# Kernel tuning notes

Measured on AMD Instinct MI355X. Metric: run time of the kernel, lower is better.

## Reference

```python
import jax, jax.numpy as jnp
import numpy as np

N_HEAD = 16
N_EMBD = 1024
BLOCK = 2048
B, T = 4, 2048


def setup_inputs() -> dict:
    key = jax.random.key(0)
    ks = jax.random.split(key, 5)
    s = 0.02
    return {
        "x": jax.random.normal(ks[0], (B, T, N_EMBD), dtype=jnp.float32),
        "qkv_w": jax.random.normal(ks[1], (3 * N_EMBD, N_EMBD), dtype=jnp.float32) * s,
        "qkv_b": jnp.zeros((3 * N_EMBD,), dtype=jnp.float32),
        "proj_w": jax.random.normal(ks[2], (N_EMBD, N_EMBD), dtype=jnp.float32) * s,
        "proj_b": jnp.zeros((N_EMBD,), dtype=jnp.float32),
    }


def reference(x, qkv_w, qkv_b, proj_w, proj_b):
    Bx, Tx, C = x.shape
    hd = C // N_HEAD
    qkv = x @ qkv_w.T + qkv_b  # [B,T,3C]
    q, k, v = jnp.split(qkv, 3, axis=-1)
    # [B,T,C] -> [B,H,T,hd]
    def heads(t):
        return t.reshape(Bx, Tx, N_HEAD, hd).transpose(0, 2, 1, 3)
    q, k, v = heads(q), heads(k), heads(v)
    scores = jnp.einsum("bhqd,bhkd->bhqk", q, k) / jnp.sqrt(jnp.float32(hd))
    causal = jnp.tril(jnp.ones((Tx, Tx), dtype=bool))
    scores = jnp.where(causal[None, None, :, :], scores, -jnp.inf)
    attn = jax.nn.softmax(scores, axis=-1)
    out = jnp.einsum("bhqk,bhkd->bhqd", attn, v)
    out = out.transpose(0, 2, 1, 3).reshape(Bx, Tx, C)
    return out @ proj_w.T + proj_b
```

## Files before the change

### kernel.cpp

```cpp
#include <hip/hip_runtime.h>
#include <stdint.h>
#include <math.h>

#define DEVI __device__ __forceinline__

typedef __attribute__((ext_vector_type(8))) short bf16x8;
typedef __attribute__((ext_vector_type(4))) float f32x4;

DEVI unsigned short f2bf(float f) {
  union { float f; unsigned u; } v; v.f = f;
  unsigned u = v.u;
  u += 0x7fffu + ((u >> 16) & 1u);
  return (unsigned short)(u >> 16);
}

DEVI unsigned cvt_pk_bf16(float a, float b) {
  unsigned r;
  asm("v_cvt_pk_bf16_f32 %0, %1, %2" : "=v"(r) : "v"(a), "v"(b));
  return r;
}

DEVI f32x4 mfma16(bf16x8 a, bf16x8 b, f32x4 c) {
  return __builtin_amdgcn_mfma_f32_16x16x32_bf16(a, b, c, 0, 0, 0);
}

DEVI void gld16(const unsigned short* g, unsigned short* l) {
  __builtin_amdgcn_global_load_lds(
      (const __attribute__((address_space(1))) unsigned int*)(uintptr_t)g,
      (__attribute__((address_space(3))) unsigned int*)(unsigned int)(uintptr_t)l,
      16, 0, 0);
}

#define VMCNT(n) asm volatile("s_waitcnt vmcnt(" #n ")" ::: "memory")
#define BAR()                              \
  do {                                     \
    __builtin_amdgcn_s_barrier();          \
    __builtin_amdgcn_sched_barrier(0);     \
  } while (0)

__global__ __launch_bounds__(256) void cvt3_kernel(
    const float* __restrict__ a, unsigned short* __restrict__ oa,
    const float* __restrict__ b, unsigned short* __restrict__ ob,
    const float* __restrict__ c, unsigned short* __restrict__ oc) {
  int bid = blockIdx.x;
  const float* in; unsigned short* out; int i;
  if (bid < 8192)       { in = a; out = oa; i = bid; }
  else if (bid < 11264) { in = b; out = ob; i = bid - 8192; }
  else                  { in = c; out = oc; i = bid - 11264; }
  int idx = (i * 256 + (int)threadIdx.x) * 4;
  float4 v = *(const float4*)(in + idx);
  unsigned lo = f2bf(v.x) | ((unsigned)f2bf(v.y) << 16);
  unsigned hi = f2bf(v.z) | ((unsigned)f2bf(v.w) << 16);
  uint2 o; o.x = lo; o.y = hi;
  *(uint2*)(out + idx) = o;
}

template <int MODE, int NBH>
__global__ __launch_bounds__(512, 2) void gemm8(
    const unsigned short* __restrict__ A, const unsigned short* __restrict__ Bw,
    const float* __restrict__ bias, float* __restrict__ Cf,
    unsigned short* __restrict__ Qo, unsigned short* __restrict__ Ko,
    unsigned short* __restrict__ Vo, int M, int N, int K, int nbx) {
  extern __shared__ unsigned short lds[];
  constexpr int BUFS = 8192 + 4096 * NBH;
  const int tid = threadIdx.x;
  const int lane = tid & 63;
  const int w = tid >> 6;
  const int wm = w >> 2, wn = w & 3;
  const int lr = lane & 15, lq = lane >> 4;

  const int cpx = gridDim.x >> 3;
  const int swz = (blockIdx.x & 7) * cpx + (blockIdx.x >> 3);
  const int bx = swz % nbx, by = swz / nbx;
  const int m0 = by * 256, n0 = bx * (NBH * 128);

  const unsigned short* pa = A + (size_t)(m0 + (lane >> 2)) * K + ((lane & 3) << 3);
  const unsigned short* pb = Bw + (size_t)(n0 + (lane >> 2)) * K + ((lane & 3) << 3);

  f32x4 acc[8][2 * NBH] = {};

  auto sA = [&](int buf, int kt, int c) {
    gld16(pa + (size_t)(c << 4) * K + kt, lds + buf * BUFS + (c << 9));
  };
  auto sB = [&](int buf, int kt, int c) {
    gld16(pb + (size_t)(c << 4) * K + kt, lds + buf * BUFS + 8192 + (c << 9));
  };
  auto stage = [&](int buf, int t) {
    const int kt = t << 5;
    sA(buf, kt, w); sA(buf, kt, 8 + w);
    sB(buf, kt, w);
    if constexpr (NBH == 2) sB(buf, kt, 8 + w);
  };

#define LDA(A_, mh)                                                          \
  _Pragma("unroll") for (int i = 0; i < 4; ++i)                              \
    A_[i] = *(const bf16x8*)(As_ + (wm * 128 + (mh) * 64 + i * 16 + lr) * 32 \
                             + lq * 8);
#define LDB(B_, nh)                                                          \
  _Pragma("unroll") for (int j = 0; j < 2; ++j)                              \
    B_[j] = *(const bf16x8*)(Bs_ + (wn * (NBH * 32) + (nh) * 32 + j * 16     \
                             + lr) * 32 + lq * 8);
#define MM(A_, B_, mh, nh)                                                   \
  __builtin_amdgcn_s_setprio(1);                                             \
  _Pragma("unroll") for (int i = 0; i < 4; ++i)                              \
    _Pragma("unroll") for (int j = 0; j < 2; ++j)                            \
      acc[(mh) * 4 + i][(nh) * 2 + j] =                                      \
          mfma16(A_[i], B_[j], acc[(mh) * 4 + i][(nh) * 2 + j]);             \
  __builtin_amdgcn_s_setprio(0);

  const int NT = K >> 5;
  stage(0, 0); stage(1, 1); stage(2, 2);
  if constexpr (NBH == 2) { VMCNT(8); } else { VMCNT(6); }
  BAR();

  for (int t = 0; t < NT; ++t) {
    if (t + 3 < NT) stage((t + 3) & 3, t + 3);
    const unsigned short* As_ = lds + (t & 3) * BUFS;
    const unsigned short* Bs_ = As_ + 8192;
    bf16x8 af0[4], af1[4], b0[2];
    if constexpr (NBH == 2) {
      bf16x8 b1[2];
      LDA(af0, 0); LDB(b0, 0);
      MM(af0, b0, 0, 0);
      LDB(b1, 1);
      MM(af0, b1, 0, 1);
      LDA(af1, 1);
      MM(af1, b1, 1, 1);
      MM(af1, b0, 1, 0);
    } else {
      LDA(af0, 0); LDB(b0, 0);
      MM(af0, b0, 0, 0);
      LDA(af1, 1);
      MM(af1, b0, 1, 0);
    }
    if (t < NT - 3) {
      if constexpr (NBH == 2) { VMCNT(8); } else { VMCNT(6); }
      BAR();
    } else if (t == NT - 3) {
      if constexpr (NBH == 2) { VMCNT(4); } else { VMCNT(3); }
      BAR();
    } else if (t == NT - 2) {
      VMCNT(0); BAR();
    }
  }
#undef LDA
#undef LDB
#undef MM

#pragma unroll
  for (int mt = 0; mt < 8; ++mt) {
#pragma unroll
    for (int nt = 0; nt < 2 * NBH; ++nt) {
      int n_g = n0 + wn * (NBH * 32) + nt * 16 + lr;
      float bv = bias[n_g];
      if (MODE == 1) {
#pragma unroll
        for (int r = 0; r < 4; ++r) {
          int m_g = m0 + wm * 128 + mt * 16 + lq * 4 + r;
          Cf[(size_t)m_g * N + n_g] = acc[mt][nt][r] + bv;
        }
      } else {
        int which = n_g >> 10;
        int rem = n_g & 1023;
        int h = rem >> 6, d = rem & 63;
        int m_base = m0 + wm * 128 + mt * 16 + lq * 4;
        int b = m_base >> 11, tt = m_base & 2047;
        if (which == 2) {
          uint2 pv;
          pv.x = cvt_pk_bf16(acc[mt][nt][0] + bv, acc[mt][nt][1] + bv);
          pv.y = cvt_pk_bf16(acc[mt][nt][2] + bv, acc[mt][nt][3] + bv);
          *(uint2*)(Vo + (((size_t)(b * 16 + h) * 64 + d) * 2048 + tt)) = pv;
        } else {
          unsigned short* p = (which == 0) ? Qo : Ko;
#pragma unroll
          for (int r = 0; r < 4; ++r) {
            size_t idx = (((size_t)(b * 16 + h) * 2048) + tt + r) * 64 + d;
            p[idx] = f2bf(acc[mt][nt][r] + bv);
          }
        }
      }
    }
  }
}

__global__ __launch_bounds__(512, 2) void attn_kernel(
    const unsigned short* __restrict__ Q, const unsigned short* __restrict__ K,
    const unsigned short* __restrict__ V, unsigned short* __restrict__ Y) {
  constexpr int T = 2048, HD = 64, H = 16;
  __shared__ unsigned short Kt[2][64 * 72];
  __shared__ unsigned short Vt[2][64 * 72];
  __shared__ unsigned short Pt[8][16 * 72];

  const int tid = threadIdx.x;
  const int lane = tid & 63;
  const int w = tid >> 6;
  const int lr = lane & 15, lq = lane >> 4;
  const int pair = blockIdx.x;
  const int h = blockIdx.y;
  const int b = blockIdx.z;
  const size_t bh = (size_t)(b * H + h) * T * HD;
  const float SC = 0.125f * 1.44269504089f;

  const int krow = tid >> 3, kcb = (tid & 7) << 3;

  float4 kr, vr;
  auto load_tile = [&](int jt) {
    const int c0 = jt * 64;
    kr = *(const float4*)(K + bh + (size_t)(c0 + krow) * HD + kcb);
    vr = *(const float4*)(V + bh + (size_t)krow * T + c0 + kcb);
  };
  auto stage = [&](int buf) {
    *(float4*)(&Kt[buf][krow * 72 + kcb]) = kr;
    *(float4*)(&Vt[buf][krow * 72 + kcb]) = vr;
  };

  load_tile(0);

  for (int phase = 0; phase < 2; ++phase) {
    const int qt = phase ? (7 - pair) : pair;
    const int q0 = qt * 256;
    const int nkv = 4 * (qt + 1);
    const int qw = q0 + w * 32;

    bf16x8 qf[2][2];
#pragma unroll
    for (int qs = 0; qs < 2; ++qs)
#pragma unroll
      for (int kb = 0; kb < 2; ++kb)
        qf[qs][kb] = *(const bf16x8*)(Q + bh + (size_t)(qw + qs * 16 + lr) * HD +
                                      kb * 32 + lq * 8);

    f32x4 o[2][4] = {};
    float mi[2] = {-INFINITY, -INFINITY}, li[2] = {0.f, 0.f};

    stage(0);
    load_tile(1);
    __syncthreads();

    for (int jt = 0; jt < nkv; ++jt) {
      const int c0 = jt * 64;
      const int buf = jt & 1;

      if (c0 <= qw + 31) {
        f32x4 s[2][4];
        __builtin_amdgcn_s_setprio(1);
#pragma unroll
        for (int nt = 0; nt < 4; ++nt) {
          bf16x8 kf0 = *(const bf16x8*)(&Kt[buf][(nt * 16 + lr) * 72 + lq * 8]);
          bf16x8 kf1 = *(const bf16x8*)(&Kt[buf][(nt * 16 + lr) * 72 + 32 + lq * 8]);
#pragma unroll
          for (int qs = 0; qs < 2; ++qs) {
            f32x4 z = {};
            z = mfma16(kf0, qf[qs][0], z);
            s[qs][nt] = mfma16(kf1, qf[qs][1], z);
          }
        }
        __builtin_amdgcn_s_setprio(0);
        if (c0 + 63 > qw) {
#pragma unroll
          for (int qs = 0; qs < 2; ++qs) {
            int qg = qw + qs * 16 + lr;
#pragma unroll
            for (int nt = 0; nt < 4; ++nt)
#pragma unroll
              for (int r = 0; r < 4; ++r) {
                int kvg = c0 + nt * 16 + lq * 4 + r;
                if (kvg > qg) s[qs][nt][r] = -INFINITY;
              }
          }
        }
        float mxs[2];
#pragma unroll
        for (int qs = 0; qs < 2; ++qs) {
          float mx = -INFINITY;
#pragma unroll
          for (int nt = 0; nt < 4; ++nt)
            mx = fmaxf(mx, fmaxf(fmaxf(s[qs][nt][0], s[qs][nt][1]),
                                 fmaxf(s[qs][nt][2], s[qs][nt][3])));
          mx = fmaxf(mx, __shfl_xor(mx, 16));
          mx = fmaxf(mx, __shfl_xor(mx, 32));
          mxs[qs] = mx * SC;
        }
        if (!__all((mxs[0] <= mi[0] + 8.f) && (mxs[1] <= mi[1] + 8.f))) {
#pragma unroll
          for (int qs = 0; qs < 2; ++qs) {
            float mnew = fmaxf(mi[qs], mxs[qs]);
            float alpha = __builtin_amdgcn_exp2f(mi[qs] - mnew);
            mi[qs] = mnew;
            li[qs] *= alpha;
#pragma unroll
            for (int nt = 0; nt < 4; ++nt)
#pragma unroll
              for (int r = 0; r < 4; ++r) o[qs][nt][r] *= alpha;
          }
        }
        bf16x8 pf[2][2];
#pragma unroll
        for (int qs = 0; qs < 2; ++qs) {
          float rs = 0.f;
#pragma unroll
          for (int nt = 0; nt < 4; ++nt) {
            float p0 = __builtin_amdgcn_exp2f(fmaf(s[qs][nt][0], SC, -mi[qs]));
            float p1 = __builtin_amdgcn_exp2f(fmaf(s[qs][nt][1], SC, -mi[qs]));
            float p2 = __builtin_amdgcn_exp2f(fmaf(s[qs][nt][2], SC, -mi[qs]));
            float p3 = __builtin_amdgcn_exp2f(fmaf(s[qs][nt][3], SC, -mi[qs]));
            rs += (p0 + p1) + (p2 + p3);
            uint2 pk;
            pk.x = cvt_pk_bf16(p0, p1);
            pk.y = cvt_pk_bf16(p2, p3);
            *(uint2*)(&Pt[w][lr * 72 + nt * 16 + lq * 4]) = pk;
          }
          li[qs] += rs;
#pragma unroll
          for (int kb = 0; kb < 2; ++kb)
            pf[qs][kb] = *(const bf16x8*)(&Pt[w][lr * 72 + kb * 32 + lq * 8]);
        }
        __builtin_amdgcn_s_setprio(1);
#pragma unroll
        for (int nt = 0; nt < 4; ++nt) {
          bf16x8 vf0 = *(const bf16x8*)(&Vt[buf][(nt * 16 + lr) * 72 + lq * 8]);
          bf16x8 vf1 = *(const bf16x8*)(&Vt[buf][(nt * 16 + lr) * 72 + 32 + lq * 8]);
#pragma unroll
          for (int qs = 0; qs < 2; ++qs) {
            o[qs][nt] = mfma16(vf0, pf[qs][0], o[qs][nt]);
            o[qs][nt] = mfma16(vf1, pf[qs][1], o[qs][nt]);
          }
        }
        __builtin_amdgcn_s_setprio(0);
      }

      if (jt + 1 < nkv) {
        stage(buf ^ 1);
        if (jt + 2 < nkv) load_tile(jt + 2);
        else if (phase == 0) load_tile(0);
        __syncthreads();
      }
    }

#pragma unroll
    for (int qs = 0; qs < 2; ++qs) {
      float l = li[qs];
      l += __shfl_xor(l, 16);
      l += __shfl_xor(l, 32);
      float inv = 1.f / l;
      int t_g = qw + qs * 16 + lr;
#pragma unroll
      for (int nt = 0; nt < 4; ++nt) {
        uint2 yv;
        yv.x = cvt_pk_bf16(o[qs][nt][0] * inv, o[qs][nt][1] * inv);
        yv.y = cvt_pk_bf16(o[qs][nt][2] * inv, o[qs][nt][3] * inv);
        *(uint2*)(Y + ((size_t)(b * T + t_g)) * 1024 + h * 64 + nt * 16 + lq * 4) = yv;
      }
    }
  }
}

extern "C" void kernel_launch(void* const* d_in, const int* in_sizes, int n_in,
                              void* d_out, int out_size, void* d_ws, size_t ws_size,
                              hipStream_t stream) {
  const float* x = (const float*)d_in[0];
  const float* qkv_w = (const float*)d_in[1];
  const float* qkv_b = (const float*)d_in[2];
  const float* proj_w = (const float*)d_in[3];
  const float* proj_b = (const float*)d_in[4];
  float* out = (float*)d_out;

  unsigned short* ws = (unsigned short*)d_ws;
  unsigned short* xb = ws;
  unsigned short* wqkv = xb + 8388608;
  unsigned short* wproj = wqkv + 3145728;
  unsigned short* Qb = wproj + 1048576;
  unsigned short* Kb = Qb + 8388608;
  unsigned short* Vb = Kb + 8388608;
  unsigned short* Yb = Vb + 8388608;

  auto* g0 = gemm8<0, 2>;
  auto* g1 = gemm8<1, 1>;
  static bool attr_set = false;
  if (!attr_set) {
    (void)hipFuncSetAttribute((const void*)g0,
                              hipFuncAttributeMaxDynamicSharedMemorySize, 131072);
    (void)hipFuncSetAttribute((const void*)g1,
                              hipFuncAttributeMaxDynamicSharedMemorySize, 98304);
    attr_set = true;
  }

  cvt3_kernel<<<12288, 256, 0, stream>>>(x, xb, qkv_w, wqkv, proj_w, wproj);

  gemm8<0, 2><<<dim3(384), 512, 131072, stream>>>(xb, wqkv, qkv_b, nullptr, Qb, Kb,
                                                  Vb, 8192, 3072, 1024, 12);
  attn_kernel<<<dim3(4, 16, 4), 512, 0, stream>>>(Qb, Kb, Vb, Yb);
  gemm8<1, 1><<<dim3(256), 512, 98304, stream>>>(Yb, wproj, proj_b, out, nullptr,
                                                 nullptr, nullptr, 8192, 1024, 1024, 8);
}
```

Before: 256.0 us.

## XOR-swizzle GEMM LDS tiles and load all fragments before MFMA block

Applies an XOR swizzle to the column chunk when staging A/B tiles into LDS via global_load_lds, with a matching swizzle on the LDS fragment reads. This is meant to reduce LDS bank conflicts on the 64-byte-row layout. It also replaces the interleaved half-tile load/MFMA schedule with loading all A and B fragments up front, then running one MFMA block, and it unifies the vmcnt waits via a template helper. Loading everything first raises register pressure and removes some overlap between LDS reads and MFMAs.

```diff
diff --git a/kernel.cpp b/kernel.cpp
--- a/kernel.cpp
+++ b/kernel.cpp
@@ -37,6 +37,15 @@
     __builtin_amdgcn_s_barrier();          \
     __builtin_amdgcn_sched_barrier(0);     \
   } while (0)
+
+template <int N> DEVI void vmcntc() {
+  static_assert(N >= 0 && N <= 12, "");
+  if constexpr (N == 0) VMCNT(0);
+  else if constexpr (N == 3) VMCNT(3);
+  else if constexpr (N == 4) VMCNT(4);
+  else if constexpr (N == 6) VMCNT(6);
+  else if constexpr (N == 8) VMCNT(8);
+}
 
 __global__ __launch_bounds__(256) void cvt3_kernel(
     const float* __restrict__ a, unsigned short* __restrict__ oa,
@@ -63,6 +72,7 @@
     unsigned short* __restrict__ Vo, int M, int N, int K, int nbx) {
   extern __shared__ unsigned short lds[];
   constexpr int BUFS = 8192 + 4096 * NBH;
+  constexpr int LPT = 2 + NBH;
   const int tid = threadIdx.x;
   const int lane = tid & 63;
   const int w = tid >> 6;
@@ -74,8 +84,12 @@
   const int bx = swz % nbx, by = swz / nbx;
   const int m0 = by * 256, n0 = bx * (NBH * 128);
 
-  const unsigned short* pa = A + (size_t)(m0 + (lane >> 2)) * K + ((lane & 3) << 3);
-  const unsigned short* pb = Bw + (size_t)(n0 + (lane >> 2)) * K + ((lane & 3) << 3);
+  const int srow = lane >> 2;
+  const int scol = (((lane & 3) ^ ((lane >> 3) & 3)) << 3);
+  const unsigned short* pa = A + (size_t)(m0 + srow) * K + scol;
+  const unsigned short* pb = Bw + (size_t)(n0 + srow) * K + scol;
+
+  const int rswz = (lq ^ ((lr >> 1) & 3)) << 3;
 
   f32x4 acc[8][2 * NBH] = {};
 
@@ -92,60 +106,36 @@
     if constexpr (NBH == 2) sB(buf, kt, 8 + w);
   };
 
-#define LDA(A_, mh)                                                          \
-  _Pragma("unroll") for (int i = 0; i < 4; ++i)                              \
-    A_[i] = *(const bf16x8*)(As_ + (wm * 128 + (mh) * 64 + i * 16 + lr) * 32 \
-                             + lq * 8);
-#define LDB(B_, nh)                                                          \
-  _Pragma("unroll") for (int j = 0; j < 2; ++j)                              \
-    B_[j] = *(const bf16x8*)(Bs_ + (wn * (NBH * 32) + (nh) * 32 + j * 16     \
-                             + lr) * 32 + lq * 8);
-#define MM(A_, B_, mh, nh)                                                   \
-  __builtin_amdgcn_s_setprio(1);                                             \
-  _Pragma("unroll") for (int i = 0; i < 4; ++i)                              \
-    _Pragma("unroll") for (int j = 0; j < 2; ++j)                            \
-      acc[(mh) * 4 + i][(nh) * 2 + j] =                                      \
-          mfma16(A_[i], B_[j], acc[(mh) * 4 + i][(nh) * 2 + j]);             \
-  __builtin_amdgcn_s_setprio(0);
-
   const int NT = K >> 5;
   stage(0, 0); stage(1, 1); stage(2, 2);
-  if constexpr (NBH == 2) { VMCNT(8); } else { VMCNT(6); }
+  vmcntc<2 * LPT>();
   BAR();
 
   for (int t = 0; t < NT; ++t) {
     if (t + 3 < NT) stage((t + 3) & 3, t + 3);
     const unsigned short* As_ = lds + (t & 3) * BUFS;
     const unsigned short* Bs_ = As_ + 8192;
-    bf16x8 af0[4], af1[4], b0[2];
-    if constexpr (NBH == 2) {
-      bf16x8 b1[2];
-      LDA(af0, 0); LDB(b0, 0);
-      MM(af0, b0, 0, 0);
-      LDB(b1, 1);
-      MM(af0, b1, 0, 1);
-      LDA(af1, 1);
-      MM(af1, b1, 1, 1);
-      MM(af1, b0, 1, 0);
-    } else {
-      LDA(af0, 0); LDB(b0, 0);
-      MM(af0, b0, 0, 0);
-      LDA(af1, 1);
-      MM(af1, b0, 1, 0);
-    }
-    if (t < NT - 3) {
-      if constexpr (NBH == 2) { VMCNT(8); } else { VMCNT(6); }
+    bf16x8 af[8], bf[2 * NBH];
+#pragma unroll
+    for (int mt = 0; mt < 8; ++mt)
+      af[mt] = *(const bf16x8*)(As_ + (wm * 128 + mt * 16 + lr) * 32 + rswz);
+#pragma unroll
+    for (int nt = 0; nt < 2 * NBH; ++nt)
+      bf[nt] = *(const bf16x8*)(Bs_ + (wn * (NBH * 32) + nt * 16 + lr) * 32 + rswz);
+    __builtin_amdgcn_s_setprio(1);
+#pragma unroll
+    for (int mt = 0; mt < 8; ++mt)
+#pragma unroll
+      for (int nt = 0; nt < 2 * NBH; ++nt)
+        acc[mt][nt] = mfma16(af[mt], bf[nt], acc[mt][nt]);
+    __builtin_amdgcn_s_setprio(0);
+    if (t + 1 < NT) {
+      if (t + 3 < NT)      vmcntc<2 * LPT>();
+      else if (t + 2 < NT) vmcntc<LPT>();
+      else                 vmcntc<0>();
       BAR();
-    } else if (t == NT - 3) {
-      if constexpr (NBH == 2) { VMCNT(4); } else { VMCNT(3); }
-      BAR();
-    } else if (t == NT - 2) {
-      VMCNT(0); BAR();
     }
   }
-#undef LDA
-#undef LDB
-#undef MM
 
 #pragma unroll
   for (int mt = 0; mt < 8; ++mt) {
```

Result: no change. 252.5 us (-1.4%).
